# Kernel optimization log

Hardware: AMD Instinct MI355X
Metric: run time of the kernel (lower is better)

## Reference

```python
import jax, jax.numpy as jnp
import numpy as np

B, S, D, E, K, H = 2, 1024, 1024, 8, 2, 2048
Z_COEF = 1e-4  # router_z_loss_coef


def setup_inputs() -> dict:
    key = jax.random.key(0)
    ks = jax.random.split(key, 9)
    std = 0.02
    return {
        "x": jax.random.normal(ks[0], (B, S, D), jnp.float32),
        "router_w": jax.random.normal(ks[1], (E, D), jnp.float32) * std,
        "router_bias": jnp.zeros((E,), jnp.float32),
        "gate_w": jax.random.normal(ks[2], (E, H, D), jnp.float32) * std,
        "up_w": jax.random.normal(ks[3], (E, H, D), jnp.float32) * std,
        "down_w": jax.random.normal(ks[4], (E, D, H), jnp.float32) * std,
        "sh_gate_w": jax.random.normal(ks[5], (H, D), jnp.float32) * std,
        "sh_up_w": jax.random.normal(ks[6], (H, D), jnp.float32) * std,
        "sh_down_w": jax.random.normal(ks[7], (D, H), jnp.float32) * std,
    }


def reference(x, router_w, router_bias, gate_w, up_w, down_w, sh_gate_w, sh_up_w, sh_down_w):
    b, s, d = x.shape
    flat = x.reshape(-1, d)                                   # [N, D]
    n_tokens = flat.shape[0]

    # ---- router ----
    logits = flat @ router_w.T                                # [N, E]
    biased = logits + jax.lax.stop_gradient(router_bias)      # bias is detached
    _, topk_idx = jax.lax.top_k(biased, K)                    # [N, K]
    topk_logits = jnp.take_along_axis(logits, topk_idx, axis=-1)
    topk_weights = jax.nn.softmax(topk_logits.astype(jnp.float32), axis=-1).astype(x.dtype)

    router_z = jax.nn.logsumexp(logits.astype(jnp.float32), axis=-1)
    router_z_loss = jnp.mean(router_z ** 2) * Z_COEF

    # ---- load-balance stats (detached in the original via no_grad) ----
    full_probs = jax.lax.stop_gradient(jax.nn.softmax(logits.astype(jnp.float32), axis=-1))
    p_i = full_probs.mean(axis=0)                             # [E]
    mask = jnp.zeros_like(full_probs).at[jnp.arange(n_tokens)[:, None], topk_idx].set(1.0)
    f_i = mask.mean(axis=0)                                   # [E]
    load_balance = jnp.sum(p_i * f_i) * E
    aux_loss = jnp.zeros((), x.dtype)                         # load_balancing == "aux_loss_free"

    # ---- routed experts ----
    # Identical math to gather(weights)[token] + SwiGLU einsum + scatter-add:
    # out[n] = sum_k w[n,k] * SwiGLU_{idx[n,k]}(x[n]), computed as E masked GEMMs
    # to avoid materializing [N*K, H, D] weight copies.
    routed = jnp.zeros_like(flat)
    for e in range(E):
        w_e = jnp.sum(topk_weights * (topk_idx == e), axis=-1)            # [N]
        h = jax.nn.silu(flat @ gate_w[e].T) * (flat @ up_w[e].T)          # [N, H]
        routed = routed + w_e[:, None] * (h @ down_w[e].T)                # [N, D]

    # ---- shared expert (num_shared_experts = 1) ----
    shared = (jax.nn.silu(flat @ sh_gate_w.T) * (flat @ sh_up_w.T)) @ sh_down_w.T

    hidden_states = (routed + shared).reshape(b, s, d)
    return hidden_states, aux_loss, router_z_loss, jax.lax.stop_gradient(load_balance)
```

## Files before the change

kernel.cpp:

```cpp
#include <hip/hip_runtime.h>

#define N_TOK 2048
#define DIM   1024
#define NE    8
#define HID   2048
#define A_SHARED 4096
#define OUT_HID (N_TOK * DIM)

typedef float v4f __attribute__((ext_vector_type(4)));
typedef short v8s __attribute__((ext_vector_type(8)));

#define OFF_XBF   0ull
#define OFF_H     4194304ull
#define OFF_TOK   29360128ull
#define OFF_WL    (OFF_TOK + 24576ull)
#define OFF_IDX   (OFF_WL + 24576ull)
#define OFF_TW    (OFF_IDX + 16384ull)
#define OFF_STATS (OFF_TW + 16384ull)

struct Stats {
  int counts[NE];
  int fill[NE];
  int offs[NE + 2];
  float z2;
  float psum[NE];
};

__device__ __forceinline__ unsigned short f2bf(float f) {
  union { float f; unsigned u; } v; v.f = f;
  unsigned r = v.u + 0x7FFFu + ((v.u >> 16) & 1u);
  return (unsigned short)(r >> 16);
}
__device__ __forceinline__ unsigned pack2bf(float a, float b) {
  return (unsigned)f2bf(a) | ((unsigned)f2bf(b) << 16);
}

__device__ __forceinline__ unsigned cvt2bf(float a, float b) {
  unsigned r;
  asm("v_cvt_pk_bf16_f32 %0, %1, %2" : "=v"(r) : "v"(a), "v"(b));
  return r;
}
__device__ __forceinline__ void st8bf(unsigned short* p, float4 a, float4 b) {
  uint4 o;
  o.x = cvt2bf(a.x, a.y);
  o.y = cvt2bf(a.z, a.w);
  o.z = cvt2bf(b.x, b.y);
  o.w = cvt2bf(b.z, b.w);
  *(uint4*)p = o;
}

__device__ __forceinline__ void async_lds16(const void* g, void* l) {
  __builtin_amdgcn_global_load_lds(
      (const __attribute__((address_space(1))) void*)g,
      (__attribute__((address_space(3))) void*)l, 16, 0, 0);
}

__global__ __launch_bounds__(256) void router_kernel(
    const float* __restrict__ x, const float* __restrict__ rw, const float* __restrict__ rb,
    unsigned short* __restrict__ xbf,
    int* __restrict__ idxbuf, float* __restrict__ twbuf, Stats* __restrict__ st) {
  int lane = threadIdx.x & 63;
  int wv = threadIdx.x >> 6;
  int n = blockIdx.x * 4 + wv;

  float acc[NE];
#pragma unroll
  for (int e = 0; e < NE; ++e) acc[e] = 0.f;

  const float4* x4 = (const float4*)(x + (size_t)n * DIM);
  uint2* xb2 = (uint2*)xbf + (size_t)n * 256;
#pragma unroll
  for (int q = 0; q < 4; ++q) {
    float4 xv = x4[q * 64 + lane];
    uint2 xo;
    xo.x = pack2bf(xv.x, xv.y);
    xo.y = pack2bf(xv.z, xv.w);
    xb2[q * 64 + lane] = xo;
#pragma unroll
    for (int e = 0; e < NE; ++e) {
      const float4* w4 = (const float4*)(rw + (size_t)e * DIM);
      float4 wvv = w4[q * 64 + lane];
      acc[e] += xv.x * wvv.x + xv.y * wvv.y + xv.z * wvv.z + xv.w * wvv.w;
    }
  }
#pragma unroll
  for (int off = 32; off; off >>= 1) {
#pragma unroll
    for (int e = 0; e < NE; ++e) acc[e] += __shfl_xor(acc[e], off);
  }

  float mx = acc[0];
#pragma unroll
  for (int e = 1; e < NE; ++e) mx = fmaxf(mx, acc[e]);
  float pr[NE];
  float es = 0.f;
#pragma unroll
  for (int e = 0; e < NE; ++e) { pr[e] = __expf(acc[e] - mx); es += pr[e]; }
  float inv = 1.f / es;
#pragma unroll
  for (int e = 0; e < NE; ++e) pr[e] *= inv;
  float z = mx + __logf(es);

  float b0 = -1e30f; int i0 = 0;
#pragma unroll
  for (int e = 0; e < NE; ++e) {
    float bb = acc[e] + rb[e];
    if (bb > b0) { b0 = bb; i0 = e; }
  }
  float b1 = -1e30f; int i1 = 0;
#pragma unroll
  for (int e = 0; e < NE; ++e) {
    if (e == i0) continue;
    float bb = acc[e] + rb[e];
    if (bb > b1) { b1 = bb; i1 = e; }
  }
  float l0 = acc[i0], l1 = acc[i1];
  float m2 = fmaxf(l0, l1);
  float e0 = __expf(l0 - m2), e1 = __expf(l1 - m2);
  float den = 1.f / (e0 + e1);
  float w0 = e0 * den, w1 = e1 * den;

  __shared__ float redp[4][9];
  __shared__ int redc[4][8];
  if (lane == 0) {
    idxbuf[n * 2] = i0; idxbuf[n * 2 + 1] = i1;
    twbuf[n * 2] = w0;  twbuf[n * 2 + 1] = w1;
#pragma unroll
    for (int e = 0; e < NE; ++e) redp[wv][e] = pr[e];
    redp[wv][8] = z * z;
#pragma unroll
    for (int e = 0; e < NE; ++e) redc[wv][e] = (e == i0) + (e == i1);
  }
  __syncthreads();
  int t = threadIdx.x;
  if (t < 9) {
    float s = redp[0][t] + redp[1][t] + redp[2][t] + redp[3][t];
    if (t < 8) atomicAdd(&st->psum[t], s);
    else       atomicAdd(&st->z2, s);
  } else if (t >= 16 && t < 24) {
    int e = t - 16;
    atomicAdd(&st->counts[e], redc[0][e] + redc[1][e] + redc[2][e] + redc[3][e]);
  }
}

__global__ void scan_kernel(Stats* __restrict__ st, float* __restrict__ out) {
  if (threadIdx.x == 0 && blockIdx.x == 0) {
    int o = 0;
#pragma unroll
    for (int e = 0; e < NE; ++e) { st->offs[e] = o; o += st->counts[e]; }
    st->offs[NE] = o;
    st->offs[NE + 1] = o + N_TOK;
    float zl = st->z2 / (float)N_TOK * 1e-4f;
    float lb = 0.f;
#pragma unroll
    for (int e = 0; e < NE; ++e)
      lb += (st->psum[e] / (float)N_TOK) * ((float)st->counts[e] / (float)N_TOK);
    lb *= (float)NE;
    out[OUT_HID + 0] = 0.f;
    out[OUT_HID + 1] = zl;
    out[OUT_HID + 2] = lb;
  }
}

__global__ __launch_bounds__(256) void scatter_kernel(
    const int* __restrict__ idxbuf, const float* __restrict__ twbuf,
    Stats* __restrict__ st, int* __restrict__ tok, float* __restrict__ wl) {
  int n = blockIdx.x * 256 + threadIdx.x;
#pragma unroll
  for (int k = 0; k < 2; ++k) {
    int e = idxbuf[n * 2 + k];
    int pos = st->offs[e] + atomicAdd(&st->fill[e], 1);
    tok[pos] = n;
    wl[pos] = twbuf[n * 2 + k];
  }
  tok[A_SHARED + n] = n;
  wl[A_SHARED + n] = 1.f;
}


__global__ __launch_bounds__(256, 2) void gateup_kernel(
    const float* __restrict__ gw, const float* __restrict__ uw,
    const float* __restrict__ shg, const float* __restrict__ shu,
    const unsigned short* __restrict__ xbf, const int* __restrict__ tok,
    const Stats* __restrict__ st, unsigned short* __restrict__ hbuf) {
  int e = blockIdx.z;
  int seg0 = st->offs[e];
  int cnt = st->offs[e + 1] - seg0;
  int m0 = blockIdx.y * 128;
  if (m0 >= cnt) return;
  int n0 = blockIdx.x * 128;

  __shared__ alignas(16) unsigned short As[2][128 * 32];
  __shared__ alignas(16) unsigned short Bg[2][128 * 32];
  __shared__ alignas(16) unsigned short Bu[2][128 * 32];

  int tid = threadIdx.x, l = tid & 63, w = tid >> 6;
  int wr = w >> 1, wc = w & 1;

  int sj = l >> 3;
  int ss = (l & 7) ^ sj;
  int grow = 2 * sj + (ss >> 2);
  int gch = ss & 3;

  const float* gbase = (e < NE) ? gw + (size_t)e * HID * DIM : shg;
  const float* ubase = (e < NE) ? uw + (size_t)e * HID * DIM : shu;

  const unsigned short* ap[2];
  const float* gp[2];
  const float* up[2];
#pragma unroll
  for (int q = 0; q < 2; ++q) {
    int row = (w * 2 + q) * 16 + grow;
    int ar = m0 + row; if (ar > cnt - 1) ar = cnt - 1;
    ap[q] = xbf + (size_t)tok[seg0 + ar] * DIM + gch * 8;
    size_t wb = (size_t)(n0 + row) * DIM + gch * 8;
    gp[q] = gbase + wb;
    up[q] = ubase + wb;
  }

  int lh = (l & 15) >> 1;
  int lofs = lh * 64 + ((((l & 1) * 4 + (l >> 4)) ^ lh) * 8);

  v4f accg[4][4], accu[4][4];
#pragma unroll
  for (int mi = 0; mi < 4; ++mi)
#pragma unroll
    for (int ni = 0; ni < 4; ++ni) {
      accg[mi][ni] = (v4f){0.f, 0.f, 0.f, 0.f};
      accu[mi][ni] = (v4f){0.f, 0.f, 0.f, 0.f};
    }

  float4 rg[2][2], ru[2][2];
#pragma unroll
  for (int q = 0; q < 2; ++q) {
    rg[q][0] = ((const float4*)gp[q])[0];
    rg[q][1] = ((const float4*)gp[q])[1];
    ru[q][0] = ((const float4*)up[q])[0];
    ru[q][1] = ((const float4*)up[q])[1];
  }
#pragma unroll
  for (int q = 0; q < 2; ++q)
    async_lds16(ap[q], &As[0][(w * 2 + q) * 512]);
#pragma unroll
  for (int q = 0; q < 2; ++q) {
    st8bf(&Bg[0][(w * 2 + q) * 512 + l * 8], rg[q][0], rg[q][1]);
    st8bf(&Bu[0][(w * 2 + q) * 512 + l * 8], ru[q][0], ru[q][1]);
  }

  int pb = 0;
  for (int k0 = 0; k0 < DIM; k0 += 32, pb ^= 1) {
    __syncthreads();

    v8s af[4], bgf[4], buf_[4];
#pragma unroll
    for (int mi = 0; mi < 4; ++mi)
      af[mi] = *(const v8s*)&As[pb][(wr * 32 + mi * 8) * 64 + lofs];
#pragma unroll
    for (int ni = 0; ni < 4; ++ni) {
      bgf[ni]  = *(const v8s*)&Bg[pb][(wc * 32 + ni * 8) * 64 + lofs];
      buf_[ni] = *(const v8s*)&Bu[pb][(wc * 32 + ni * 8) * 64 + lofs];
    }

    int nb = pb ^ 1;
    int kn = k0 + 32;
    if (kn < DIM) {
#pragma unroll
      for (int q = 0; q < 2; ++q) {
        rg[q][0] = ((const float4*)(gp[q] + kn))[0];
        rg[q][1] = ((const float4*)(gp[q] + kn))[1];
        ru[q][0] = ((const float4*)(up[q] + kn))[0];
        ru[q][1] = ((const float4*)(up[q] + kn))[1];
      }
#pragma unroll
      for (int q = 0; q < 2; ++q)
        async_lds16(ap[q] + kn, &As[nb][(w * 2 + q) * 512]);
    }

#pragma unroll
    for (int mi = 0; mi < 4; ++mi)
#pragma unroll
      for (int ni = 0; ni < 4; ++ni) {
        accg[mi][ni] = __builtin_amdgcn_mfma_f32_16x16x32_bf16(af[mi], bgf[ni], accg[mi][ni], 0, 0, 0);
        accu[mi][ni] = __builtin_amdgcn_mfma_f32_16x16x32_bf16(af[mi], buf_[ni], accu[mi][ni], 0, 0, 0);
      }

    if (kn < DIM) {
#pragma unroll
      for (int q = 0; q < 2; ++q) {
        st8bf(&Bg[nb][(w * 2 + q) * 512 + l * 8], rg[q][0], rg[q][1]);
        st8bf(&Bu[nb][(w * 2 + q) * 512 + l * 8], ru[q][0], ru[q][1]);
      }
    }
  }

  int col = l & 15, rq = (l >> 4) * 4;
#pragma unroll
  for (int mi = 0; mi < 4; ++mi) {
#pragma unroll
    for (int rr = 0; rr < 4; ++rr) {
      int rl = wr * 64 + mi * 16 + rq + rr;
      if (m0 + rl < cnt) {
        size_t rowb = (size_t)(seg0 + m0 + rl) * HID + n0 + wc * 64;
#pragma unroll
        for (int ni = 0; ni < 4; ++ni) {
          float g = accg[mi][ni][rr], u = accu[mi][ni][rr];
          hbuf[rowb + ni * 16 + col] = f2bf(g * u / (1.f + __expf(-g)));
        }
      }
    }
  }
}

__global__ __launch_bounds__(256, 2) void down_kernel(
    const float* __restrict__ dw, const float* __restrict__ shd,
    const unsigned short* __restrict__ hbuf,
    const int* __restrict__ tok, const float* __restrict__ wl,
    const Stats* __restrict__ st, float* __restrict__ out) {
  int e = blockIdx.z;
  int seg0 = st->offs[e];
  int cnt = st->offs[e + 1] - seg0;
  int m0 = blockIdx.y * 128;
  if (m0 >= cnt) return;
  int n0 = blockIdx.x * 128;

  __shared__ alignas(16) unsigned short As[2][128 * 32];
  __shared__ alignas(16) unsigned short Bs[2][128 * 32];

  int tid = threadIdx.x, l = tid & 63, w = tid >> 6;
  int wr = w >> 1, wc = w & 1;

  int sj = l >> 3;
  int ss = (l & 7) ^ sj;
  int grow = 2 * sj + (ss >> 2);
  int gch = ss & 3;

  const float* dbase = (e < NE) ? dw + (size_t)e * DIM * HID : shd;

  const unsigned short* ap[2];
  const float* bp[2];
#pragma unroll
  for (int q = 0; q < 2; ++q) {
    int row = (w * 2 + q) * 16 + grow;
    int ar = m0 + row; if (ar > cnt - 1) ar = cnt - 1;
    ap[q] = hbuf + (size_t)(seg0 + ar) * HID + gch * 8;
    bp[q] = dbase + (size_t)(n0 + row) * HID + gch * 8;
  }

  int lh = (l & 15) >> 1;
  int lofs = lh * 64 + ((((l & 1) * 4 + (l >> 4)) ^ lh) * 8);

  v4f acc[4][4];
#pragma unroll
  for (int mi = 0; mi < 4; ++mi)
#pragma unroll
    for (int ni = 0; ni < 4; ++ni) acc[mi][ni] = (v4f){0.f, 0.f, 0.f, 0.f};

  float4 rb_[2][2];
#pragma unroll
  for (int q = 0; q < 2; ++q) {
    rb_[q][0] = ((const float4*)bp[q])[0];
    rb_[q][1] = ((const float4*)bp[q])[1];
  }
#pragma unroll
  for (int q = 0; q < 2; ++q)
    async_lds16(ap[q], &As[0][(w * 2 + q) * 512]);
#pragma unroll
  for (int q = 0; q < 2; ++q)
    st8bf(&Bs[0][(w * 2 + q) * 512 + l * 8], rb_[q][0], rb_[q][1]);

  int pb = 0;
  for (int k0 = 0; k0 < HID; k0 += 32, pb ^= 1) {
    __syncthreads();

    v8s af[4], bf[4];
#pragma unroll
    for (int mi = 0; mi < 4; ++mi)
      af[mi] = *(const v8s*)&As[pb][(wr * 32 + mi * 8) * 64 + lofs];
#pragma unroll
    for (int ni = 0; ni < 4; ++ni)
      bf[ni] = *(const v8s*)&Bs[pb][(wc * 32 + ni * 8) * 64 + lofs];

    int nb = pb ^ 1;
    int kn = k0 + 32;
    if (kn < HID) {
#pragma unroll
      for (int q = 0; q < 2; ++q) {
        rb_[q][0] = ((const float4*)(bp[q] + kn))[0];
        rb_[q][1] = ((const float4*)(bp[q] + kn))[1];
      }
#pragma unroll
      for (int q = 0; q < 2; ++q)
        async_lds16(ap[q] + kn, &As[nb][(w * 2 + q) * 512]);
    }

#pragma unroll
    for (int mi = 0; mi < 4; ++mi)
#pragma unroll
      for (int ni = 0; ni < 4; ++ni)
        acc[mi][ni] = __builtin_amdgcn_mfma_f32_16x16x32_bf16(af[mi], bf[ni], acc[mi][ni], 0, 0, 0);

    if (kn < HID) {
#pragma unroll
      for (int q = 0; q < 2; ++q)
        st8bf(&Bs[nb][(w * 2 + q) * 512 + l * 8], rb_[q][0], rb_[q][1]);
    }
  }

  int col = l & 15, rq = (l >> 4) * 4;
#pragma unroll
  for (int mi = 0; mi < 4; ++mi) {
#pragma unroll
    for (int rr = 0; rr < 4; ++rr) {
      int rl = wr * 64 + mi * 16 + rq + rr;
      if (m0 + rl < cnt) {
        int t = tok[seg0 + m0 + rl];
        float wgt = wl[seg0 + m0 + rl];
        float* ob = out + (size_t)t * DIM + n0 + wc * 64;
#pragma unroll
        for (int ni = 0; ni < 4; ++ni)
          atomicAdd(ob + ni * 16 + col, acc[mi][ni][rr] * wgt);
      }
    }
  }
}

extern "C" void kernel_launch(void* const* d_in, const int* in_sizes, int n_in,
                              void* d_out, int out_size, void* d_ws, size_t ws_size,
                              hipStream_t stream) {
  const float* x   = (const float*)d_in[0];
  const float* rw  = (const float*)d_in[1];
  const float* rb  = (const float*)d_in[2];
  const float* gw  = (const float*)d_in[3];
  const float* uw  = (const float*)d_in[4];
  const float* dw  = (const float*)d_in[5];
  const float* shg = (const float*)d_in[6];
  const float* shu = (const float*)d_in[7];
  const float* shd = (const float*)d_in[8];
  float* out = (float*)d_out;
  char* ws = (char*)d_ws;

  unsigned short* xbf  = (unsigned short*)(ws + OFF_XBF);
  unsigned short* hbuf = (unsigned short*)(ws + OFF_H);
  int*   tok  = (int*)(ws + OFF_TOK);
  float* wl   = (float*)(ws + OFF_WL);
  int*   idxb = (int*)(ws + OFF_IDX);
  float* twb  = (float*)(ws + OFF_TW);
  Stats* st   = (Stats*)(ws + OFF_STATS);

  hipMemsetAsync(d_out, 0, (size_t)out_size * sizeof(float), stream);
  hipMemsetAsync(st, 0, sizeof(Stats), stream);

  router_kernel<<<512, 256, 0, stream>>>(x, rw, rb, xbf, idxb, twb, st);
  scan_kernel<<<1, 64, 0, stream>>>(st, out);
  scatter_kernel<<<8, 256, 0, stream>>>(idxb, twb, st, tok, wl);
  gateup_kernel<<<dim3(16, 16, 9), 256, 0, stream>>>(gw, uw, shg, shu, xbf, tok, st, hbuf);
  down_kernel<<<dim3(8, 16, 9), 256, 0, stream>>>(dw, shd, hbuf, tok, wl, st, out);
}
```

Measured before the change: 446.9 us.

## Halve M tile to 64 rows and split down-projection K across two blocks

Reduces the token-row tile of both expert GEMMs from 128 to 64 rows. The down-projection also splits its hidden reduction into two halves, and each half atomically adds its partial result into the output. This creates more blocks per expert to fill the GPU when per-expert token counts are small. In exchange, the fp32 weights are re-read and converted to bf16 about twice as often, per-block MFMA work is smaller, and the extra atomics on the output add contention.

```diff
diff --git a/kernel.cpp b/kernel.cpp
--- a/kernel.cpp
+++ b/kernel.cpp
@@ -186,11 +186,11 @@
   int e = blockIdx.z;
   int seg0 = st->offs[e];
   int cnt = st->offs[e + 1] - seg0;
-  int m0 = blockIdx.y * 128;
+  int m0 = blockIdx.y * 64;
   if (m0 >= cnt) return;
   int n0 = blockIdx.x * 128;
 
-  __shared__ alignas(16) unsigned short As[2][128 * 32];
+  __shared__ alignas(16) unsigned short As[2][64 * 32];
   __shared__ alignas(16) unsigned short Bg[2][128 * 32];
   __shared__ alignas(16) unsigned short Bu[2][128 * 32];
 
@@ -205,14 +205,15 @@
   const float* gbase = (e < NE) ? gw + (size_t)e * HID * DIM : shg;
   const float* ubase = (e < NE) ? uw + (size_t)e * HID * DIM : shu;
 
-  const unsigned short* ap[2];
+  int arow = w * 16 + grow;
+  int ar = m0 + arow; if (ar > cnt - 1) ar = cnt - 1;
+  const unsigned short* ap = xbf + (size_t)tok[seg0 + ar] * DIM + gch * 8;
+
   const float* gp[2];
   const float* up[2];
 #pragma unroll
   for (int q = 0; q < 2; ++q) {
     int row = (w * 2 + q) * 16 + grow;
-    int ar = m0 + row; if (ar > cnt - 1) ar = cnt - 1;
-    ap[q] = xbf + (size_t)tok[seg0 + ar] * DIM + gch * 8;
     size_t wb = (size_t)(n0 + row) * DIM + gch * 8;
     gp[q] = gbase + wb;
     up[q] = ubase + wb;
@@ -221,9 +222,9 @@
   int lh = (l & 15) >> 1;
   int lofs = lh * 64 + ((((l & 1) * 4 + (l >> 4)) ^ lh) * 8);
 
-  v4f accg[4][4], accu[4][4];
-#pragma unroll
-  for (int mi = 0; mi < 4; ++mi)
+  v4f accg[2][4], accu[2][4];
+#pragma unroll
+  for (int mi = 0; mi < 2; ++mi)
 #pragma unroll
     for (int ni = 0; ni < 4; ++ni) {
       accg[mi][ni] = (v4f){0.f, 0.f, 0.f, 0.f};
@@ -238,9 +239,7 @@
     ru[q][0] = ((const float4*)up[q])[0];
     ru[q][1] = ((const float4*)up[q])[1];
   }
-#pragma unroll
-  for (int q = 0; q < 2; ++q)
-    async_lds16(ap[q], &As[0][(w * 2 + q) * 512]);
+  async_lds16(ap, &As[0][w * 512]);
 #pragma unroll
   for (int q = 0; q < 2; ++q) {
     st8bf(&Bg[0][(w * 2 + q) * 512 + l * 8], rg[q][0], rg[q][1]);
@@ -251,10 +250,10 @@
   for (int k0 = 0; k0 < DIM; k0 += 32, pb ^= 1) {
     __syncthreads();
 
-    v8s af[4], bgf[4], buf_[4];
-#pragma unroll
-    for (int mi = 0; mi < 4; ++mi)
-      af[mi] = *(const v8s*)&As[pb][(wr * 32 + mi * 8) * 64 + lofs];
+    v8s af[2], bgf[4], buf_[4];
+#pragma unroll
+    for (int mi = 0; mi < 2; ++mi)
+      af[mi] = *(const v8s*)&As[pb][(wr * 16 + mi * 8) * 64 + lofs];
 #pragma unroll
     for (int ni = 0; ni < 4; ++ni) {
       bgf[ni]  = *(const v8s*)&Bg[pb][(wc * 32 + ni * 8) * 64 + lofs];
@@ -271,13 +270,11 @@
         ru[q][0] = ((const float4*)(up[q] + kn))[0];
         ru[q][1] = ((const float4*)(up[q] + kn))[1];
       }
-#pragma unroll
-      for (int q = 0; q < 2; ++q)
-        async_lds16(ap[q] + kn, &As[nb][(w * 2 + q) * 512]);
-    }
-
-#pragma unroll
-    for (int mi = 0; mi < 4; ++mi)
+      async_lds16(ap + kn, &As[nb][w * 512]);
+    }
+
+#pragma unroll
+    for (int mi = 0; mi < 2; ++mi)
 #pragma unroll
       for (int ni = 0; ni < 4; ++ni) {
         accg[mi][ni] = __builtin_amdgcn_mfma_f32_16x16x32_bf16(af[mi], bgf[ni], accg[mi][ni], 0, 0, 0);
@@ -295,10 +292,10 @@
 
   int col = l & 15, rq = (l >> 4) * 4;
 #pragma unroll
-  for (int mi = 0; mi < 4; ++mi) {
+  for (int mi = 0; mi < 2; ++mi) {
 #pragma unroll
     for (int rr = 0; rr < 4; ++rr) {
-      int rl = wr * 64 + mi * 16 + rq + rr;
+      int rl = wr * 32 + mi * 16 + rq + rr;
       if (m0 + rl < cnt) {
         size_t rowb = (size_t)(seg0 + m0 + rl) * HID + n0 + wc * 64;
 #pragma unroll
@@ -311,19 +308,22 @@
   }
 }
 
+#define KSPL (HID / 2)
 __global__ __launch_bounds__(256, 2) void down_kernel(
     const float* __restrict__ dw, const float* __restrict__ shd,
     const unsigned short* __restrict__ hbuf,
     const int* __restrict__ tok, const float* __restrict__ wl,
     const Stats* __restrict__ st, float* __restrict__ out) {
-  int e = blockIdx.z;
+  int zz = blockIdx.z;
+  int e = zz >> 1;
+  int kb = (zz & 1) * KSPL;
   int seg0 = st->offs[e];
   int cnt = st->offs[e + 1] - seg0;
-  int m0 = blockIdx.y * 128;
+  int m0 = blockIdx.y * 64;
   if (m0 >= cnt) return;
   int n0 = blockIdx.x * 128;
 
-  __shared__ alignas(16) unsigned short As[2][128 * 32];
+  __shared__ alignas(16) unsigned short As[2][64 * 32];
   __shared__ alignas(16) unsigned short Bs[2][128 * 32];
 
   int tid = threadIdx.x, l = tid & 63, w = tid >> 6;
@@ -336,22 +336,23 @@
 
   const float* dbase = (e < NE) ? dw + (size_t)e * DIM * HID : shd;
 
-  const unsigned short* ap[2];
+  int arow = w * 16 + grow;
+  int ar = m0 + arow; if (ar > cnt - 1) ar = cnt - 1;
+  const unsigned short* ap = hbuf + (size_t)(seg0 + ar) * HID + gch * 8 + kb;
+
   const float* bp[2];
 #pragma unroll
   for (int q = 0; q < 2; ++q) {
     int row = (w * 2 + q) * 16 + grow;
-    int ar = m0 + row; if (ar > cnt - 1) ar = cnt - 1;
-    ap[q] = hbuf + (size_t)(seg0 + ar) * HID + gch * 8;
-    bp[q] = dbase + (size_t)(n0 + row) * HID + gch * 8;
+    bp[q] = dbase + (size_t)(n0 + row) * HID + gch * 8 + kb;
   }
 
   int lh = (l & 15) >> 1;
   int lofs = lh * 64 + ((((l & 1) * 4 + (l >> 4)) ^ lh) * 8);
 
-  v4f acc[4][4];
-#pragma unroll
-  for (int mi = 0; mi < 4; ++mi)
+  v4f acc[2][4];
+#pragma unroll
+  for (int mi = 0; mi < 2; ++mi)
 #pragma unroll
     for (int ni = 0; ni < 4; ++ni) acc[mi][ni] = (v4f){0.f, 0.f, 0.f, 0.f};
 
@@ -361,45 +362,41 @@
     rb_[q][0] = ((const float4*)bp[q])[0];
     rb_[q][1] = ((const float4*)bp[q])[1];
   }
-#pragma unroll
-  for (int q = 0; q < 2; ++q)
-    async_lds16(ap[q], &As[0][(w * 2 + q) * 512]);
+  async_lds16(ap, &As[0][w * 512]);
 #pragma unroll
   for (int q = 0; q < 2; ++q)
     st8bf(&Bs[0][(w * 2 + q) * 512 + l * 8], rb_[q][0], rb_[q][1]);
 
   int pb = 0;
-  for (int k0 = 0; k0 < HID; k0 += 32, pb ^= 1) {
+  for (int k0 = 0; k0 < KSPL; k0 += 32, pb ^= 1) {
     __syncthreads();
 
-    v8s af[4], bf[4];
-#pragma unroll
-    for (int mi = 0; mi < 4; ++mi)
-      af[mi] = *(const v8s*)&As[pb][(wr * 32 + mi * 8) * 64 + lofs];
+    v8s af[2], bf[4];
+#pragma unroll
+    for (int mi = 0; mi < 2; ++mi)
+      af[mi] = *(const v8s*)&As[pb][(wr * 16 + mi * 8) * 64 + lofs];
 #pragma unroll
     for (int ni = 0; ni < 4; ++ni)
       bf[ni] = *(const v8s*)&Bs[pb][(wc * 32 + ni * 8) * 64 + lofs];
 
     int nb = pb ^ 1;
     int kn = k0 + 32;
-    if (kn < HID) {
+    if (kn < KSPL) {
 #pragma unroll
       for (int q = 0; q < 2; ++q) {
         rb_[q][0] = ((const float4*)(bp[q] + kn))[0];
         rb_[q][1] = ((const float4*)(bp[q] + kn))[1];
       }
-#pragma unroll
-      for (int q = 0; q < 2; ++q)
-        async_lds16(ap[q] + kn, &As[nb][(w * 2 + q) * 512]);
-    }
-
-#pragma unroll
-    for (int mi = 0; mi < 4; ++mi)
+      async_lds16(ap + kn, &As[nb][w * 512]);
+    }
+
+#pragma unroll
+    for (int mi = 0; mi < 2; ++mi)
 #pragma unroll
       for (int ni = 0; ni < 4; ++ni)
         acc[mi][ni] = __builtin_amdgcn_mfma_f32_16x16x32_bf16(af[mi], bf[ni], acc[mi][ni], 0, 0, 0);
 
-    if (kn < HID) {
+    if (kn < KSPL) {
 #pragma unroll
       for (int q = 0; q < 2; ++q)
         st8bf(&Bs[nb][(w * 2 + q) * 512 + l * 8], rb_[q][0], rb_[q][1]);
@@ -408,10 +405,10 @@
 
   int col = l & 15, rq = (l >> 4) * 4;
 #pragma unroll
-  for (int mi = 0; mi < 4; ++mi) {
+  for (int mi = 0; mi < 2; ++mi) {
 #pragma unroll
     for (int rr = 0; rr < 4; ++rr) {
-      int rl = wr * 64 + mi * 16 + rq + rr;
+      int rl = wr * 32 + mi * 16 + rq + rr;
       if (m0 + rl < cnt) {
         int t = tok[seg0 + m0 + rl];
         float wgt = wl[seg0 + m0 + rl];
@@ -453,6 +450,6 @@
   router_kernel<<<512, 256, 0, stream>>>(x, rw, rb, xbf, idxb, twb, st);
   scan_kernel<<<1, 64, 0, stream>>>(st, out);
   scatter_kernel<<<8, 256, 0, stream>>>(idxb, twb, st, tok, wl);
-  gateup_kernel<<<dim3(16, 16, 9), 256, 0, stream>>>(gw, uw, shg, shu, xbf, tok, st, hbuf);
-  down_kernel<<<dim3(8, 16, 9), 256, 0, stream>>>(dw, shd, hbuf, tok, wl, st, out);
-}
+  gateup_kernel<<<dim3(16, 32, 9), 256, 0, stream>>>(gw, uw, shg, shu, xbf, tok, st, hbuf);
+  down_kernel<<<dim3(8, 32, 18), 256, 0, stream>>>(dw, shd, hbuf, tok, wl, st, out);
+}
```

Result: no change. 439.9 us (-1.6%).

## Enlarge GEMM M-tile to 256 with 512 threads and split-K the down projection

Applied to the files above, without the earlier changes.

Both expert GEMM kernels now use 512-thread blocks covering 256 token rows by 128 output columns. Each fp32 weight tile is loaded and converted to bf16 once per 256 tokens instead of once per 128, which halves global weight traffic and conversion work. The down projection also splits its 2048-long reduction into two halves on separate blocks, since the output is already accumulated with atomics, to recover the parallelism lost to fewer M tiles. The costs are more atomic adds on the output, more LDS per block, and more wasted rows when an expert's token count is not a multiple of 256.

```diff
diff --git a/kernel.cpp b/kernel.cpp
--- a/kernel.cpp
+++ b/kernel.cpp
@@ -178,7 +178,7 @@
 }
 
 
-__global__ __launch_bounds__(256, 2) void gateup_kernel(
+__global__ __launch_bounds__(512, 2) void gateup_kernel(
     const float* __restrict__ gw, const float* __restrict__ uw,
     const float* __restrict__ shg, const float* __restrict__ shu,
     const unsigned short* __restrict__ xbf, const int* __restrict__ tok,
@@ -186,11 +186,11 @@
   int e = blockIdx.z;
   int seg0 = st->offs[e];
   int cnt = st->offs[e + 1] - seg0;
-  int m0 = blockIdx.y * 128;
+  int m0 = blockIdx.y * 256;
   if (m0 >= cnt) return;
   int n0 = blockIdx.x * 128;
 
-  __shared__ alignas(16) unsigned short As[2][128 * 32];
+  __shared__ alignas(16) unsigned short As[2][256 * 32];
   __shared__ alignas(16) unsigned short Bg[2][128 * 32];
   __shared__ alignas(16) unsigned short Bu[2][128 * 32];
 
@@ -206,17 +206,16 @@
   const float* ubase = (e < NE) ? uw + (size_t)e * HID * DIM : shu;
 
   const unsigned short* ap[2];
-  const float* gp[2];
-  const float* up[2];
 #pragma unroll
   for (int q = 0; q < 2; ++q) {
     int row = (w * 2 + q) * 16 + grow;
     int ar = m0 + row; if (ar > cnt - 1) ar = cnt - 1;
     ap[q] = xbf + (size_t)tok[seg0 + ar] * DIM + gch * 8;
-    size_t wb = (size_t)(n0 + row) * DIM + gch * 8;
-    gp[q] = gbase + wb;
-    up[q] = ubase + wb;
-  }
+  }
+
+  int brow = w * 16 + grow;
+  const float* gp = gbase + (size_t)(n0 + brow) * DIM + gch * 8;
+  const float* up = ubase + (size_t)(n0 + brow) * DIM + gch * 8;
 
   int lh = (l & 15) >> 1;
   int lofs = lh * 64 + ((((l & 1) * 4 + (l >> 4)) ^ lh) * 8);
@@ -230,22 +229,16 @@
       accu[mi][ni] = (v4f){0.f, 0.f, 0.f, 0.f};
     }
 
-  float4 rg[2][2], ru[2][2];
-#pragma unroll
-  for (int q = 0; q < 2; ++q) {
-    rg[q][0] = ((const float4*)gp[q])[0];
-    rg[q][1] = ((const float4*)gp[q])[1];
-    ru[q][0] = ((const float4*)up[q])[0];
-    ru[q][1] = ((const float4*)up[q])[1];
-  }
+  float4 rg[2], ru[2];
+  rg[0] = ((const float4*)gp)[0];
+  rg[1] = ((const float4*)gp)[1];
+  ru[0] = ((const float4*)up)[0];
+  ru[1] = ((const float4*)up)[1];
 #pragma unroll
   for (int q = 0; q < 2; ++q)
     async_lds16(ap[q], &As[0][(w * 2 + q) * 512]);
-#pragma unroll
-  for (int q = 0; q < 2; ++q) {
-    st8bf(&Bg[0][(w * 2 + q) * 512 + l * 8], rg[q][0], rg[q][1]);
-    st8bf(&Bu[0][(w * 2 + q) * 512 + l * 8], ru[q][0], ru[q][1]);
-  }
+  st8bf(&Bg[0][w * 512 + l * 8], rg[0], rg[1]);
+  st8bf(&Bu[0][w * 512 + l * 8], ru[0], ru[1]);
 
   int pb = 0;
   for (int k0 = 0; k0 < DIM; k0 += 32, pb ^= 1) {
@@ -264,13 +257,10 @@
     int nb = pb ^ 1;
     int kn = k0 + 32;
     if (kn < DIM) {
-#pragma unroll
-      for (int q = 0; q < 2; ++q) {
-        rg[q][0] = ((const float4*)(gp[q] + kn))[0];
-        rg[q][1] = ((const float4*)(gp[q] + kn))[1];
-        ru[q][0] = ((const float4*)(up[q] + kn))[0];
-        ru[q][1] = ((const float4*)(up[q] + kn))[1];
-      }
+      rg[0] = ((const float4*)(gp + kn))[0];
+      rg[1] = ((const float4*)(gp + kn))[1];
+      ru[0] = ((const float4*)(up + kn))[0];
+      ru[1] = ((const float4*)(up + kn))[1];
 #pragma unroll
       for (int q = 0; q < 2; ++q)
         async_lds16(ap[q] + kn, &As[nb][(w * 2 + q) * 512]);
@@ -285,11 +275,8 @@
       }
 
     if (kn < DIM) {
-#pragma unroll
-      for (int q = 0; q < 2; ++q) {
-        st8bf(&Bg[nb][(w * 2 + q) * 512 + l * 8], rg[q][0], rg[q][1]);
-        st8bf(&Bu[nb][(w * 2 + q) * 512 + l * 8], ru[q][0], ru[q][1]);
-      }
+      st8bf(&Bg[nb][w * 512 + l * 8], rg[0], rg[1]);
+      st8bf(&Bu[nb][w * 512 + l * 8], ru[0], ru[1]);
     }
   }
 
@@ -303,27 +290,30 @@
         size_t rowb = (size_t)(seg0 + m0 + rl) * HID + n0 + wc * 64;
 #pragma unroll
         for (int ni = 0; ni < 4; ++ni) {
-          float g = accg[mi][ni][rr], u = accu[mi][ni][rr];
-          hbuf[rowb + ni * 16 + col] = f2bf(g * u / (1.f + __expf(-g)));
+          float gg = accg[mi][ni][rr], u = accu[mi][ni][rr];
+          hbuf[rowb + ni * 16 + col] = f2bf(gg * u / (1.f + __expf(-gg)));
         }
       }
     }
   }
 }
 
-__global__ __launch_bounds__(256, 2) void down_kernel(
+#define KSPL (HID / 2)
+__global__ __launch_bounds__(512, 2) void down_kernel(
     const float* __restrict__ dw, const float* __restrict__ shd,
     const unsigned short* __restrict__ hbuf,
     const int* __restrict__ tok, const float* __restrict__ wl,
     const Stats* __restrict__ st, float* __restrict__ out) {
-  int e = blockIdx.z;
+  int zz = blockIdx.z;
+  int e = zz >> 1;
+  int kb = (zz & 1) * KSPL;
   int seg0 = st->offs[e];
   int cnt = st->offs[e + 1] - seg0;
-  int m0 = blockIdx.y * 128;
+  int m0 = blockIdx.y * 256;
   if (m0 >= cnt) return;
   int n0 = blockIdx.x * 128;
 
-  __shared__ alignas(16) unsigned short As[2][128 * 32];
+  __shared__ alignas(16) unsigned short As[2][256 * 32];
   __shared__ alignas(16) unsigned short Bs[2][128 * 32];
 
   int tid = threadIdx.x, l = tid & 63, w = tid >> 6;
@@ -337,14 +327,15 @@
   const float* dbase = (e < NE) ? dw + (size_t)e * DIM * HID : shd;
 
   const unsigned short* ap[2];
-  const float* bp[2];
 #pragma unroll
   for (int q = 0; q < 2; ++q) {
     int row = (w * 2 + q) * 16 + grow;
     int ar = m0 + row; if (ar > cnt - 1) ar = cnt - 1;
-    ap[q] = hbuf + (size_t)(seg0 + ar) * HID + gch * 8;
-    bp[q] = dbase + (size_t)(n0 + row) * HID + gch * 8;
-  }
+    ap[q] = hbuf + (size_t)(seg0 + ar) * HID + gch * 8 + kb;
+  }
+
+  int brow = w * 16 + grow;
+  const float* bp = dbase + (size_t)(n0 + brow) * HID + gch * 8 + kb;
 
   int lh = (l & 15) >> 1;
   int lofs = lh * 64 + ((((l & 1) * 4 + (l >> 4)) ^ lh) * 8);
@@ -355,21 +346,16 @@
 #pragma unroll
     for (int ni = 0; ni < 4; ++ni) acc[mi][ni] = (v4f){0.f, 0.f, 0.f, 0.f};
 
-  float4 rb_[2][2];
-#pragma unroll
-  for (int q = 0; q < 2; ++q) {
-    rb_[q][0] = ((const float4*)bp[q])[0];
-    rb_[q][1] = ((const float4*)bp[q])[1];
-  }
+  float4 rb_[2];
+  rb_[0] = ((const float4*)bp)[0];
+  rb_[1] = ((const float4*)bp)[1];
 #pragma unroll
   for (int q = 0; q < 2; ++q)
     async_lds16(ap[q], &As[0][(w * 2 + q) * 512]);
-#pragma unroll
-  for (int q = 0; q < 2; ++q)
-    st8bf(&Bs[0][(w * 2 + q) * 512 + l * 8], rb_[q][0], rb_[q][1]);
+  st8bf(&Bs[0][w * 512 + l * 8], rb_[0], rb_[1]);
 
   int pb = 0;
-  for (int k0 = 0; k0 < HID; k0 += 32, pb ^= 1) {
+  for (int k0 = 0; k0 < KSPL; k0 += 32, pb ^= 1) {
     __syncthreads();
 
     v8s af[4], bf[4];
@@ -382,12 +368,9 @@
 
     int nb = pb ^ 1;
     int kn = k0 + 32;
-    if (kn < HID) {
-#pragma unroll
-      for (int q = 0; q < 2; ++q) {
-        rb_[q][0] = ((const float4*)(bp[q] + kn))[0];
-        rb_[q][1] = ((const float4*)(bp[q] + kn))[1];
-      }
+    if (kn < KSPL) {
+      rb_[0] = ((const float4*)(bp + kn))[0];
+      rb_[1] = ((const float4*)(bp + kn))[1];
 #pragma unroll
       for (int q = 0; q < 2; ++q)
         async_lds16(ap[q] + kn, &As[nb][(w * 2 + q) * 512]);
@@ -399,11 +382,8 @@
       for (int ni = 0; ni < 4; ++ni)
         acc[mi][ni] = __builtin_amdgcn_mfma_f32_16x16x32_bf16(af[mi], bf[ni], acc[mi][ni], 0, 0, 0);
 
-    if (kn < HID) {
-#pragma unroll
-      for (int q = 0; q < 2; ++q)
-        st8bf(&Bs[nb][(w * 2 + q) * 512 + l * 8], rb_[q][0], rb_[q][1]);
-    }
+    if (kn < KSPL)
+      st8bf(&Bs[nb][w * 512 + l * 8], rb_[0], rb_[1]);
   }
 
   int col = l & 15, rq = (l >> 4) * 4;
@@ -453,6 +433,6 @@
   router_kernel<<<512, 256, 0, stream>>>(x, rw, rb, xbf, idxb, twb, st);
   scan_kernel<<<1, 64, 0, stream>>>(st, out);
   scatter_kernel<<<8, 256, 0, stream>>>(idxb, twb, st, tok, wl);
-  gateup_kernel<<<dim3(16, 16, 9), 256, 0, stream>>>(gw, uw, shg, shu, xbf, tok, st, hbuf);
-  down_kernel<<<dim3(8, 16, 9), 256, 0, stream>>>(dw, shd, hbuf, tok, wl, st, out);
-}
+  gateup_kernel<<<dim3(16, 8, 9), 512, 0, stream>>>(gw, uw, shg, shu, xbf, tok, st, hbuf);
+  down_kernel<<<dim3(8, 8, 18), 512, 0, stream>>>(dw, shd, hbuf, tok, wl, st, out);
+}
```

Result: no change. 447.5 us (+0.1%).
